# Performance work log

Hardware: AMD Instinct MI355X
Metric: run time of the kernel (lower is better)

Reference implementation:

```python
import jax, jax.numpy as jnp
import numpy as np

IN_DIM = 256
NUM_HEADS = 8
HEAD_DIM = IN_DIM // NUM_HEADS


def setup_inputs() -> dict:
    key = jax.random.key(0)
    k1, k2, k3, k4, k5, k6 = jax.random.split(key, 6)
    B, C, H, W = 2, IN_DIM, 64, 64
    scale = 1.0 / np.sqrt(IN_DIM)
    return {
        "tgt": jax.random.normal(k1, (B, C, H, W), dtype=jnp.float32),
        "src": jax.random.normal(k2, (B, C, H, W), dtype=jnp.float32),
        # nn.Linear weights stored as [out, in] (torch convention); y = x @ W.T
        "Wq": jax.random.normal(k3, (IN_DIM, IN_DIM), dtype=jnp.float32) * scale,
        "Wk": jax.random.normal(k4, (IN_DIM, IN_DIM), dtype=jnp.float32) * scale,
        "Wv": jax.random.normal(k5, (IN_DIM, IN_DIM), dtype=jnp.float32) * scale,
        "Wo": jax.random.normal(k6, (IN_DIM, IN_DIM), dtype=jnp.float32) * scale,
    }


def reference(tgt, src, Wq, Wk, Wv, Wo):
    B, C, H, W = src.shape
    N = H * W
    # b c h w -> b (h w) c
    src_t = src.reshape(B, C, N).transpose(0, 2, 1)
    tgt_t = tgt.reshape(B, C, N).transpose(0, 2, 1)
    # project and split heads: [B, N, C] -> [B, heads, N, head_dim]
    def heads(x, Wt):
        y = jnp.einsum('bnc,dc->bnd', x, Wt)
        return y.reshape(B, N, NUM_HEADS, HEAD_DIM).transpose(0, 2, 1, 3)
    q = heads(tgt_t, Wq)
    k = heads(src_t, Wk)
    v = heads(src_t, Wv)
    scores = jnp.einsum('bhqd,bhkd->bhqk', q, k) / jnp.sqrt(jnp.float32(HEAD_DIM))
    attn = jax.nn.softmax(scores, axis=-1)
    weighted = jnp.einsum('bhqk,bhkd->bhqd', attn, v)  # [B, heads, N, head_dim]
    weighted = weighted.transpose(0, 2, 1, 3).reshape(B, N, C)
    out = jnp.einsum('bnc,dc->bnd', weighted + tgt_t, Wo)
    return out
```

## Files before the change

kernel.cpp:

```cpp
#include <hip/hip_runtime.h>
#include <hip/hip_bf16.h>

#define IN_DIM 256
#define NHEADS 8
#define HDIM 32
#define BATCH 2
#define NTOK 4096
#define QSCALE (0.17677669529663687f * 1.4426950408889634f)

typedef __hip_bfloat16 bf16;
typedef __attribute__((ext_vector_type(8))) short bf16x8;
typedef __attribute__((ext_vector_type(4))) short bf16x4;
typedef __attribute__((ext_vector_type(4))) float f32x4;

union bfrag { bf16x8 v; bf16x4 h[2]; };

__device__ __forceinline__ float b2f(bf16 x) { return __bfloat162float(x); }

#if __has_builtin(__builtin_amdgcn_exp2f)
__device__ __forceinline__ float fast_exp2(float x) { return __builtin_amdgcn_exp2f(x); }
#else
__device__ __forceinline__ float fast_exp2(float x) { return exp2f(x); }
#endif

__device__ __forceinline__ unsigned packbf2(float a, float b) {
    union { __hip_bfloat162 h; unsigned u; } c;
    c.h = __float22bfloat162_rn(float2{a, b});
    return c.u;
}

#if __has_builtin(__builtin_amdgcn_mfma_f32_16x16x16bf16_1k)
__device__ __forceinline__ f32x4 mfma16(bf16x4 a, bf16x4 b, f32x4 c) {
    return __builtin_amdgcn_mfma_f32_16x16x16bf16_1k(a, b, c, 0, 0, 0);
}
#else
__device__ __forceinline__ f32x4 mfma16(bf16x4 a, bf16x4 b, f32x4 c) {
    bf16x8 az = {a[0], a[1], a[2], a[3], 0, 0, 0, 0};
    bf16x8 bz = {b[0], b[1], b[2], b[3], 0, 0, 0, 0};
    return __builtin_amdgcn_mfma_f32_16x16x32_bf16(az, bz, c, 0, 0, 0);
}
#endif

__device__ __forceinline__ void pack16(float4 a, float4 b, float4 c, float4 d,
                                       bf16* dst) {
    uint2 w0 = {packbf2(a.x, a.y), packbf2(a.z, a.w)};
    uint2 w1 = {packbf2(b.x, b.y), packbf2(b.z, b.w)};
    uint2 w2 = {packbf2(c.x, c.y), packbf2(c.z, c.w)};
    uint2 w3 = {packbf2(d.x, d.y), packbf2(d.z, d.w)};
    *(uint2*)(dst + 0)  = w0;
    *(uint2*)(dst + 4)  = w1;
    *(uint2*)(dst + 8)  = w2;
    *(uint2*)(dst + 12) = w3;
}

__global__ __launch_bounds__(256) void proj_mfma(
    const float* __restrict__ tgt, const float* __restrict__ src,
    const float* __restrict__ Wq, const float* __restrict__ Wk,
    const float* __restrict__ Wv,
    bf16* __restrict__ Qo, bf16* __restrict__ Ko, bf16* __restrict__ Vo)
{
    const int which = blockIdx.y;
    const int dh = blockIdx.z;
    const int b  = blockIdx.x >> 7;
    const int n0 = (blockIdx.x & 127) * 32;
    const float* X = (which == 0) ? tgt : src;
    const float* W = (which == 0) ? Wq : (which == 1 ? Wk : Wv);

    const int tid = threadIdx.x;
    const int wave = tid >> 6, lane = tid & 63;
    const int lg = lane >> 4, lc = lane & 15;
    const int wn = wave & 1, wdq = wave >> 1;

    __shared__ bf16 As[32 * 260];
    __shared__ bf16 Ws[2][128 * 36];

    {
        const float* Xb = X + (size_t)b * IN_DIM * NTOK + n0;
        for (int it = 0; it < 8; ++it) {
            int idx = it * 256 + tid;
            int c = idx >> 3, j4 = idx & 7;
            float4 x = *(const float4*)(Xb + (size_t)c * NTOK + j4 * 4);
            As[(j4 * 4 + 0) * 260 + c] = __float2bfloat16(x.x);
            As[(j4 * 4 + 1) * 260 + c] = __float2bfloat16(x.y);
            As[(j4 * 4 + 2) * 260 + c] = __float2bfloat16(x.z);
            As[(j4 * 4 + 3) * 260 + c] = __float2bfloat16(x.w);
        }
    }
    const int wd = tid >> 1, wc = (tid & 1) * 16;
    const float* Wbase = W + (size_t)(dh * 128 + wd) * IN_DIM + wc;
    {
        float4 a = *(const float4*)(Wbase + 0);
        float4 bb = *(const float4*)(Wbase + 4);
        float4 cc = *(const float4*)(Wbase + 8);
        float4 dd = *(const float4*)(Wbase + 12);
        pack16(a, bb, cc, dd, &Ws[0][wd * 36 + wc]);
    }
    __syncthreads();

    f32x4 acc[4];
    #pragma unroll
    for (int t = 0; t < 4; ++t) acc[t] = f32x4{0.f, 0.f, 0.f, 0.f};

    for (int s = 0; s < 8; ++s) {
        const int c0 = s * 32;
        float4 pa, pb, pc, pd;
        if (s < 7) {
            const float* wn_ = Wbase + (s + 1) * 32;
            pa = *(const float4*)(wn_ + 0);
            pb = *(const float4*)(wn_ + 4);
            pc = *(const float4*)(wn_ + 8);
            pd = *(const float4*)(wn_ + 12);
        }
        bfrag af;
        const bf16* ap = &As[(wn * 16 + lc) * 260 + c0 + lg * 8];
        af.h[0] = *(const bf16x4*)ap;
        af.h[1] = *(const bf16x4*)(ap + 4);
        #pragma unroll
        for (int t = 0; t < 4; ++t) {
            bfrag wf;
            const bf16* wp = &Ws[s & 1][(wdq * 64 + t * 16 + lc) * 36 + lg * 8];
            wf.h[0] = *(const bf16x4*)wp;
            wf.h[1] = *(const bf16x4*)(wp + 4);
            acc[t] = __builtin_amdgcn_mfma_f32_16x16x32_bf16(af.v, wf.v, acc[t], 0, 0, 0);
        }
        if (s < 7) {
            __syncthreads();
            pack16(pa, pb, pc, pd, &Ws[(s + 1) & 1][wd * 36 + wc]);
            __syncthreads();
        }
    }

    const int nb = n0 + wn * 16 + lg * 4;
    if (which == 2) {
        #pragma unroll
        for (int t = 0; t < 4; ++t) {
            int d = dh * 128 + wdq * 64 + t * 16 + lc;
            uint2 pk;
            pk.x = packbf2(acc[t][0], acc[t][1]);
            pk.y = packbf2(acc[t][2], acc[t][3]);
            *(uint2*)(Vo + ((size_t)b * IN_DIM + d) * NTOK + nb) = pk;
        }
    } else {
        const float sc = (which == 0) ? QSCALE : 1.0f;
        bf16* O = (which == 0) ? Qo : Ko;
        #pragma unroll
        for (int t = 0; t < 4; ++t)
            #pragma unroll
            for (int r = 0; r < 4; ++r)
                O[((size_t)b * NTOK + nb + r) * IN_DIM + dh * 128 + wdq * 64 + t * 16 + lc]
                    = __float2bfloat16(acc[t][r] * sc);
    }
}

__global__ __launch_bounds__(256) void attn_mfma_kernel(
    const bf16* __restrict__ Q, const bf16* __restrict__ K,
    const bf16* __restrict__ Vt, const float* __restrict__ tgt,
    bf16* __restrict__ Wt)
{
    const int blk = blockIdx.x;
    const int bh  = 2 * (blk & 7) + ((blk >> 3) & 1);
    const int qb  = blk >> 4;
    const int b = bh >> 3, h = bh & 7;
    const int tid  = threadIdx.x;
    const int wave = tid >> 6;
    const int lane = tid & 63;
    const int lg = lane >> 4, lc = lane & 15;
    const int qw = qb * 128 + wave * 32;

    __shared__ bf16 KL[2][64 * 40];
    __shared__ bf16 VL[2][32 * 72];

    const bf16x8 qfa = *(const bf16x8*)(Q + ((size_t)b * NTOK + qw + lc) * IN_DIM
                                          + h * HDIM + lg * 8);
    const bf16x8 qfb = *(const bf16x8*)(Q + ((size_t)b * NTOK + qw + 16 + lc) * IN_DIM
                                          + h * HDIM + lg * 8);

    bf16x4 ones4;
    #pragma unroll
    for (int i = 0; i < 4; ++i) ((short*)&ones4)[i] = (short)0x3F80;
    const f32x4 z = {0.f, 0.f, 0.f, 0.f};

    const int srow = tid >> 2, sd = (tid & 3) * 8;
    const int vrow = tid >> 3, vch = tid & 7;
    const int kwoff = srow * 40 + sd;
    const int vwoff = vrow * 72 + vch * 8;
    const int kroff = lc * 40 + lg * 8;
    const int vroff0 = lc * 72 + lg * 4;
    const int vroff1 = (16 + lc) * 72 + lg * 4;

    const bf16* Kp = K  + ((size_t)b * NTOK + srow) * IN_DIM + h * HDIM + sd;
    const bf16* Vp = Vt + ((size_t)b * IN_DIM + h * HDIM + vrow) * NTOK + vch * 8;

    f32x4 o0a = {0.f,0.f,0.f,0.f}, o1a = {0.f,0.f,0.f,0.f}, ola = {0.f,0.f,0.f,0.f};
    f32x4 o0b = {0.f,0.f,0.f,0.f}, o1b = {0.f,0.f,0.f,0.f}, olb = {0.f,0.f,0.f,0.f};

    bf16x8 kreg = *(const bf16x8*)Kp;
    bf16x8 vreg = *(const bf16x8*)Vp;
    Kp += (size_t)64 * IN_DIM;
    Vp += 64;

#define HALF(CUR)                                                              \
    {                                                                          \
        *(bf16x8*)&KL[CUR][kwoff] = kreg;                                      \
        *(bf16x8*)&VL[CUR][vwoff] = vreg;                                      \
        kreg = *(const bf16x8*)Kp;                                             \
        vreg = *(const bf16x8*)Vp;                                             \
        Kp += (size_t)64 * IN_DIM;                                             \
        Vp += 64;                                                              \
        __syncthreads();                                                       \
        bf16x8 kf[4];                                                          \
        _Pragma("unroll")                                                      \
        for (int t = 0; t < 4; ++t)                                            \
            kf[t] = *(const bf16x8*)&KL[CUR][kroff + t * 640];                 \
        bf16x4 v0[4], v1[4];                                                   \
        _Pragma("unroll")                                                      \
        for (int t = 0; t < 4; ++t) {                                          \
            v0[t] = *(const bf16x4*)&VL[CUR][vroff0 + t * 16];                 \
            v1[t] = *(const bf16x4*)&VL[CUR][vroff1 + t * 16];                 \
        }                                                                      \
        f32x4 sa[4], sb[4];                                                    \
        __builtin_amdgcn_s_setprio(1);                                         \
        _Pragma("unroll")                                                      \
        for (int t = 0; t < 4; ++t) {                                          \
            sa[t] = __builtin_amdgcn_mfma_f32_16x16x32_bf16(kf[t], qfa, z, 0,0,0); \
            sb[t] = __builtin_amdgcn_mfma_f32_16x16x32_bf16(kf[t], qfb, z, 0,0,0); \
        }                                                                      \
        __builtin_amdgcn_s_setprio(0);                                         \
        _Pragma("unroll")                                                      \
        for (int t = 0; t < 4; ++t) {                                          \
            union { bf16x4 h; uint2 u; } pka, pkb;                             \
            pka.u.x = packbf2(fast_exp2(sa[t][0]), fast_exp2(sa[t][1]));       \
            pka.u.y = packbf2(fast_exp2(sa[t][2]), fast_exp2(sa[t][3]));       \
            pkb.u.x = packbf2(fast_exp2(sb[t][0]), fast_exp2(sb[t][1]));       \
            pkb.u.y = packbf2(fast_exp2(sb[t][2]), fast_exp2(sb[t][3]));       \
            __builtin_amdgcn_s_setprio(1);                                     \
            o0a = mfma16(pka.h, v0[t], o0a);                                   \
            o1a = mfma16(pka.h, v1[t], o1a);                                   \
            ola = mfma16(pka.h, ones4, ola);                                   \
            o0b = mfma16(pkb.h, v0[t], o0b);                                   \
            o1b = mfma16(pkb.h, v1[t], o1b);                                   \
            olb = mfma16(pkb.h, ones4, olb);                                   \
            __builtin_amdgcn_s_setprio(0);                                     \
        }                                                                      \
    }

    for (int it = 0; it < NTOK / 128; ++it) {
        HALF(0)
        HALF(1)
    }
#undef HALF

    const float* tga = tgt + ((size_t)b * IN_DIM + h * HDIM + lc) * NTOK + qw + lg * 4;
    float4 r0a = *(const float4*)tga;
    float4 r1a = *(const float4*)(tga + (size_t)16 * NTOK);
    float4 r0b = *(const float4*)(tga + 16);
    float4 r1b = *(const float4*)(tga + (size_t)16 * NTOK + 16);

    bf16* opa = Wt + ((size_t)b * NTOK + qw + lg * 4) * IN_DIM + h * HDIM + lc;
    bf16* opb = opa + (size_t)16 * IN_DIM;
    #pragma unroll
    for (int r = 0; r < 4; ++r) {
        float inva = 1.f / ola[r];
        float invb = 1.f / olb[r];
        opa[(size_t)r * IN_DIM]      = __float2bfloat16(o0a[r] * inva + (&r0a.x)[r]);
        opa[(size_t)r * IN_DIM + 16] = __float2bfloat16(o1a[r] * inva + (&r1a.x)[r]);
        opb[(size_t)r * IN_DIM]      = __float2bfloat16(o0b[r] * invb + (&r0b.x)[r]);
        opb[(size_t)r * IN_DIM + 16] = __float2bfloat16(o1b[r] * invb + (&r1b.x)[r]);
    }
}

__global__ __launch_bounds__(256) void out_mfma(
    const bf16* __restrict__ A, const float* __restrict__ Wo,
    float* __restrict__ out)
{
    const int dh = blockIdx.y;
    const int b  = blockIdx.x >> 7;
    const int n0 = (blockIdx.x & 127) * 32;

    const int tid = threadIdx.x;
    const int wave = tid >> 6, lane = tid & 63;
    const int lg = lane >> 4, lc = lane & 15;
    const int wn = wave & 1, wdq = wave >> 1;

    __shared__ bf16 As[32 * 260];
    __shared__ bf16 Ws[2][128 * 36];

    {
        const bf16* Ab = A + ((size_t)b * NTOK + n0) * IN_DIM;
        for (int it = 0; it < 4; ++it) {
            int idx = it * 256 + tid;
            int r = idx >> 5, ch = idx & 31;
            bfrag v;
            v.v = *(const bf16x8*)(Ab + (size_t)r * IN_DIM + ch * 8);
            *(bf16x4*)&As[r * 260 + ch * 8]     = v.h[0];
            *(bf16x4*)&As[r * 260 + ch * 8 + 4] = v.h[1];
        }
    }
    const int wd = tid >> 1, wc = (tid & 1) * 16;
    const float* Wbase = Wo + (size_t)(dh * 128 + wd) * IN_DIM + wc;
    {
        float4 a = *(const float4*)(Wbase + 0);
        float4 bb = *(const float4*)(Wbase + 4);
        float4 cc = *(const float4*)(Wbase + 8);
        float4 dd = *(const float4*)(Wbase + 12);
        pack16(a, bb, cc, dd, &Ws[0][wd * 36 + wc]);
    }
    __syncthreads();

    f32x4 acc[4];
    #pragma unroll
    for (int t = 0; t < 4; ++t) acc[t] = f32x4{0.f, 0.f, 0.f, 0.f};

    for (int s = 0; s < 8; ++s) {
        const int c0 = s * 32;
        float4 pa, pb, pc, pd;
        if (s < 7) {
            const float* wn_ = Wbase + (s + 1) * 32;
            pa = *(const float4*)(wn_ + 0);
            pb = *(const float4*)(wn_ + 4);
            pc = *(const float4*)(wn_ + 8);
            pd = *(const float4*)(wn_ + 12);
        }
        bfrag af;
        const bf16* ap = &As[(wn * 16 + lc) * 260 + c0 + lg * 8];
        af.h[0] = *(const bf16x4*)ap;
        af.h[1] = *(const bf16x4*)(ap + 4);
        #pragma unroll
        for (int t = 0; t < 4; ++t) {
            bfrag wf;
            const bf16* wp = &Ws[s & 1][(wdq * 64 + t * 16 + lc) * 36 + lg * 8];
            wf.h[0] = *(const bf16x4*)wp;
            wf.h[1] = *(const bf16x4*)(wp + 4);
            acc[t] = __builtin_amdgcn_mfma_f32_16x16x32_bf16(af.v, wf.v, acc[t], 0, 0, 0);
        }
        if (s < 7) {
            __syncthreads();
            pack16(pa, pb, pc, pd, &Ws[(s + 1) & 1][wd * 36 + wc]);
            __syncthreads();
        }
    }

    const int nb = n0 + wn * 16 + lg * 4;
    #pragma unroll
    for (int t = 0; t < 4; ++t)
        #pragma unroll
        for (int r = 0; r < 4; ++r)
            out[((size_t)b * NTOK + nb + r) * IN_DIM + dh * 128 + wdq * 64 + t * 16 + lc]
                = acc[t][r];
}

extern "C" void kernel_launch(void* const* d_in, const int* in_sizes, int n_in,
                              void* d_out, int out_size, void* d_ws, size_t ws_size,
                              hipStream_t stream) {
    const float* tgt = (const float*)d_in[0];
    const float* src = (const float*)d_in[1];
    const float* Wq  = (const float*)d_in[2];
    const float* Wk  = (const float*)d_in[3];
    const float* Wv  = (const float*)d_in[4];
    const float* Wo  = (const float*)d_in[5];
    float* out = (float*)d_out;

    const size_t SZ = (size_t)BATCH * NTOK * IN_DIM * sizeof(bf16);
    char* w = (char*)d_ws;
    bf16* Qb  = (bf16*)(w);
    bf16* Kb  = (bf16*)(w + SZ);
    bf16* Vtb = (bf16*)(w + 2 * SZ);
    bf16* Wt  = (bf16*)(w + 3 * SZ);

    proj_mfma<<<dim3(256, 3, 2), 256, 0, stream>>>(tgt, src, Wq, Wk, Wv, Qb, Kb, Vtb);

    attn_mfma_kernel<<<512, 256, 0, stream>>>(Qb, Kb, Vtb, tgt, Wt);

    out_mfma<<<dim3(256, 2), 256, 0, stream>>>(Wt, Wo, out);
}
```

Measured before the change: 100.9 us.

## Replace LDS K/V staging with per-wave register double-buffering and wider PV MFMAs

Each wave now loads its K and V fragments straight from global memory into two register buffers, which removes the shared-memory staging and the block barrier on every 64-key step. The loads for the next tile are issued before the compute on the current one. The P·V and row-sum products now use the 16x16x32 bf16 MFMA, packing two 16-key exp tiles per operand, so they need half as many matrix instructions as the 16x16x16 path. In exchange, the four waves in a block fetch the same K/V data separately, relying on the caches, and register pressure rises. The last prefetch also reads past the end of the K/V tiles.

```diff
diff --git a/kernel.cpp b/kernel.cpp
--- a/kernel.cpp
+++ b/kernel.cpp
@@ -28,18 +28,6 @@
     c.h = __float22bfloat162_rn(float2{a, b});
     return c.u;
 }
-
-#if __has_builtin(__builtin_amdgcn_mfma_f32_16x16x16bf16_1k)
-__device__ __forceinline__ f32x4 mfma16(bf16x4 a, bf16x4 b, f32x4 c) {
-    return __builtin_amdgcn_mfma_f32_16x16x16bf16_1k(a, b, c, 0, 0, 0);
-}
-#else
-__device__ __forceinline__ f32x4 mfma16(bf16x4 a, bf16x4 b, f32x4 c) {
-    bf16x8 az = {a[0], a[1], a[2], a[3], 0, 0, 0, 0};
-    bf16x8 bz = {b[0], b[1], b[2], b[3], 0, 0, 0, 0};
-    return __builtin_amdgcn_mfma_f32_16x16x32_bf16(az, bz, c, 0, 0, 0);
-}
-#endif
 
 __device__ __forceinline__ void pack16(float4 a, float4 b, float4 c, float4 d,
                                        bf16* dst) {
@@ -167,88 +155,89 @@
     const int lg = lane >> 4, lc = lane & 15;
     const int qw = qb * 128 + wave * 32;
 
-    __shared__ bf16 KL[2][64 * 40];
-    __shared__ bf16 VL[2][32 * 72];
-
     const bf16x8 qfa = *(const bf16x8*)(Q + ((size_t)b * NTOK + qw + lc) * IN_DIM
                                           + h * HDIM + lg * 8);
     const bf16x8 qfb = *(const bf16x8*)(Q + ((size_t)b * NTOK + qw + 16 + lc) * IN_DIM
                                           + h * HDIM + lg * 8);
 
-    bf16x4 ones4;
-    #pragma unroll
-    for (int i = 0; i < 4; ++i) ((short*)&ones4)[i] = (short)0x3F80;
+    bf16x8 ones8;
+    #pragma unroll
+    for (int i = 0; i < 8; ++i) ((short*)&ones8)[i] = (short)0x3F80;
     const f32x4 z = {0.f, 0.f, 0.f, 0.f};
 
-    const int srow = tid >> 2, sd = (tid & 3) * 8;
-    const int vrow = tid >> 3, vch = tid & 7;
-    const int kwoff = srow * 40 + sd;
-    const int vwoff = vrow * 72 + vch * 8;
-    const int kroff = lc * 40 + lg * 8;
-    const int vroff0 = lc * 72 + lg * 4;
-    const int vroff1 = (16 + lc) * 72 + lg * 4;
-
-    const bf16* Kp = K  + ((size_t)b * NTOK + srow) * IN_DIM + h * HDIM + sd;
-    const bf16* Vp = Vt + ((size_t)b * IN_DIM + h * HDIM + vrow) * NTOK + vch * 8;
+    const bf16* Kr = K  + ((size_t)b * NTOK + lc) * IN_DIM + h * HDIM + lg * 8;
+    const bf16* V0 = Vt + ((size_t)b * IN_DIM + h * HDIM + lc) * NTOK + lg * 4;
+    const bf16* V1 = V0 + (size_t)16 * NTOK;
 
     f32x4 o0a = {0.f,0.f,0.f,0.f}, o1a = {0.f,0.f,0.f,0.f}, ola = {0.f,0.f,0.f,0.f};
     f32x4 o0b = {0.f,0.f,0.f,0.f}, o1b = {0.f,0.f,0.f,0.f}, olb = {0.f,0.f,0.f,0.f};
 
-    bf16x8 kreg = *(const bf16x8*)Kp;
-    bf16x8 vreg = *(const bf16x8*)Vp;
-    Kp += (size_t)64 * IN_DIM;
-    Vp += 64;
-
-#define HALF(CUR)                                                              \
+    bf16x8 kA[4], kB[4];
+    bf16x4 vA0[4], vA1[4], vB0[4], vB1[4];
+
+    const bf16* Kp = Kr;
+    const bf16* V0p = V0;
+    const bf16* V1p = V1;
+
+#define LOADSET(KS, VS0, VS1)                                                  \
     {                                                                          \
-        *(bf16x8*)&KL[CUR][kwoff] = kreg;                                      \
-        *(bf16x8*)&VL[CUR][vwoff] = vreg;                                      \
-        kreg = *(const bf16x8*)Kp;                                             \
-        vreg = *(const bf16x8*)Vp;                                             \
-        Kp += (size_t)64 * IN_DIM;                                             \
-        Vp += 64;                                                              \
-        __syncthreads();                                                       \
-        bf16x8 kf[4];                                                          \
         _Pragma("unroll")                                                      \
         for (int t = 0; t < 4; ++t)                                            \
-            kf[t] = *(const bf16x8*)&KL[CUR][kroff + t * 640];                 \
-        bf16x4 v0[4], v1[4];                                                   \
+            KS[t] = *(const bf16x8*)(Kp + (size_t)(t * 16) * IN_DIM);          \
         _Pragma("unroll")                                                      \
-        for (int t = 0; t < 4; ++t) {                                          \
-            v0[t] = *(const bf16x4*)&VL[CUR][vroff0 + t * 16];                 \
-            v1[t] = *(const bf16x4*)&VL[CUR][vroff1 + t * 16];                 \
+        for (int m = 0; m < 4; ++m) {                                          \
+            VS0[m] = *(const bf16x4*)(V0p + m * 16);                           \
+            VS1[m] = *(const bf16x4*)(V1p + m * 16);                           \
         }                                                                      \
+        Kp  += (size_t)64 * IN_DIM;                                            \
+        V0p += 64;                                                             \
+        V1p += 64;                                                             \
+    }
+
+#define COMPUTE(KS, VS0, VS1)                                                  \
+    {                                                                          \
         f32x4 sa[4], sb[4];                                                    \
         __builtin_amdgcn_s_setprio(1);                                         \
         _Pragma("unroll")                                                      \
         for (int t = 0; t < 4; ++t) {                                          \
-            sa[t] = __builtin_amdgcn_mfma_f32_16x16x32_bf16(kf[t], qfa, z, 0,0,0); \
-            sb[t] = __builtin_amdgcn_mfma_f32_16x16x32_bf16(kf[t], qfb, z, 0,0,0); \
+            sa[t] = __builtin_amdgcn_mfma_f32_16x16x32_bf16(KS[t], qfa, z, 0,0,0); \
+            sb[t] = __builtin_amdgcn_mfma_f32_16x16x32_bf16(KS[t], qfb, z, 0,0,0); \
         }                                                                      \
         __builtin_amdgcn_s_setprio(0);                                         \
         _Pragma("unroll")                                                      \
-        for (int t = 0; t < 4; ++t) {                                          \
-            union { bf16x4 h; uint2 u; } pka, pkb;                             \
-            pka.u.x = packbf2(fast_exp2(sa[t][0]), fast_exp2(sa[t][1]));       \
-            pka.u.y = packbf2(fast_exp2(sa[t][2]), fast_exp2(sa[t][3]));       \
-            pkb.u.x = packbf2(fast_exp2(sb[t][0]), fast_exp2(sb[t][1]));       \
-            pkb.u.y = packbf2(fast_exp2(sb[t][2]), fast_exp2(sb[t][3]));       \
+        for (int tcp = 0; tcp < 2; ++tcp) {                                    \
+            union { bf16x8 v; uint4 u; } pa, pb;                               \
+            pa.u.x = packbf2(fast_exp2(sa[2*tcp][0]), fast_exp2(sa[2*tcp][1]));     \
+            pa.u.y = packbf2(fast_exp2(sa[2*tcp][2]), fast_exp2(sa[2*tcp][3]));     \
+            pa.u.z = packbf2(fast_exp2(sa[2*tcp+1][0]), fast_exp2(sa[2*tcp+1][1])); \
+            pa.u.w = packbf2(fast_exp2(sa[2*tcp+1][2]), fast_exp2(sa[2*tcp+1][3])); \
+            pb.u.x = packbf2(fast_exp2(sb[2*tcp][0]), fast_exp2(sb[2*tcp][1]));     \
+            pb.u.y = packbf2(fast_exp2(sb[2*tcp][2]), fast_exp2(sb[2*tcp][3]));     \
+            pb.u.z = packbf2(fast_exp2(sb[2*tcp+1][0]), fast_exp2(sb[2*tcp+1][1])); \
+            pb.u.w = packbf2(fast_exp2(sb[2*tcp+1][2]), fast_exp2(sb[2*tcp+1][3])); \
+            bfrag B0, B1;                                                      \
+            B0.h[0] = VS0[2*tcp]; B0.h[1] = VS0[2*tcp+1];                      \
+            B1.h[0] = VS1[2*tcp]; B1.h[1] = VS1[2*tcp+1];                      \
             __builtin_amdgcn_s_setprio(1);                                     \
-            o0a = mfma16(pka.h, v0[t], o0a);                                   \
-            o1a = mfma16(pka.h, v1[t], o1a);                                   \
-            ola = mfma16(pka.h, ones4, ola);                                   \
-            o0b = mfma16(pkb.h, v0[t], o0b);                                   \
-            o1b = mfma16(pkb.h, v1[t], o1b);                                   \
-            olb = mfma16(pkb.h, ones4, olb);                                   \
+            o0a = __builtin_amdgcn_mfma_f32_16x16x32_bf16(pa.v, B0.v, o0a, 0,0,0); \
+            o1a = __builtin_amdgcn_mfma_f32_16x16x32_bf16(pa.v, B1.v, o1a, 0,0,0); \
+            ola = __builtin_amdgcn_mfma_f32_16x16x32_bf16(pa.v, ones8, ola, 0,0,0); \
+            o0b = __builtin_amdgcn_mfma_f32_16x16x32_bf16(pb.v, B0.v, o0b, 0,0,0); \
+            o1b = __builtin_amdgcn_mfma_f32_16x16x32_bf16(pb.v, B1.v, o1b, 0,0,0); \
+            olb = __builtin_amdgcn_mfma_f32_16x16x32_bf16(pb.v, ones8, olb, 0,0,0); \
             __builtin_amdgcn_s_setprio(0);                                     \
         }                                                                      \
     }
 
+    LOADSET(kA, vA0, vA1)
     for (int it = 0; it < NTOK / 128; ++it) {
-        HALF(0)
-        HALF(1)
-    }
-#undef HALF
+        LOADSET(kB, vB0, vB1)
+        COMPUTE(kA, vA0, vA1)
+        LOADSET(kA, vA0, vA1)
+        COMPUTE(kB, vB0, vB1)
+    }
+#undef LOADSET
+#undef COMPUTE
 
     const float* tga = tgt + ((size_t)b * IN_DIM + h * HDIM + lc) * NTOK + qw + lg * 4;
     float4 r0a = *(const float4*)tga;
```

Result: slower. 206.6 us (+104.7%).
